# Kernel tuning notes

Hardware: AMD Instinct MI355X
Metric: run time of the kernel (lower is better)

Reference implementation:

```python
import jax, jax.numpy as jnp
import numpy as np

SIGMA = 0.2


def setup_inputs() -> dict:
    key = jax.random.key(0)
    ks = jax.random.split(key, 16)
    N = 200000
    corner = jax.random.normal(ks[0], (N, 9), dtype=jnp.float32)
    normal = jax.random.normal(ks[1], (N, 3), dtype=jnp.float32)
    neighbour = jax.random.randint(ks[2], (N, 3), 0, N, dtype=jnp.int32)
    # Face_Rotate_Conv params: Conv1d(1,32,6,stride=3), Linear(32,64), Linear(64,64)
    conv_w = jax.random.normal(ks[3], (32, 1, 6), dtype=jnp.float32) * 0.3
    conv_b = jax.random.normal(ks[4], (32,), dtype=jnp.float32) * 0.1
    l3_w = jax.random.normal(ks[5], (64, 32), dtype=jnp.float32) * 0.15
    l3_b = jax.random.normal(ks[6], (64,), dtype=jnp.float32) * 0.05
    l4_w = jax.random.normal(ks[7], (64, 64), dtype=jnp.float32) * 0.12
    l4_b = jax.random.normal(ks[8], (64,), dtype=jnp.float32) * 0.05
    # Kernel_Correlation params: theta ~ U(0,pi), phi ~ U(0,2pi), shape [1,64,4]
    theta = jax.random.uniform(ks[9], (1, 64, 4), dtype=jnp.float32) * np.float32(np.pi)
    phi = jax.random.uniform(ks[10], (1, 64, 4), dtype=jnp.float32) * np.float32(2 * np.pi)
    # trailing 1x1 conv / bn / 1x1 conv on 131 channels
    c1_w = jax.random.normal(ks[11], (131, 131, 1), dtype=jnp.float32) * 0.08
    c1_b = jax.random.normal(ks[12], (131,), dtype=jnp.float32) * 0.05
    c2_w = jax.random.normal(ks[13], (131, 131, 1), dtype=jnp.float32) * 0.08
    c2_b = jax.random.normal(ks[14], (131,), dtype=jnp.float32) * 0.05
    bn_g = jnp.ones((131,), dtype=jnp.float32)
    bn_b = jnp.zeros((131,), dtype=jnp.float32)
    return {"corner": corner, "normal": normal, "neighbour": neighbour,
            "conv_w": conv_w, "conv_b": conv_b, "l3_w": l3_w, "l3_b": l3_b,
            "l4_w": l4_w, "l4_b": l4_b, "theta": theta, "phi": phi,
            "c1_w": c1_w, "c1_b": c1_b, "c2_w": c2_w, "c2_b": c2_b,
            "bn_g": bn_g, "bn_b": bn_b}


def reference(corner, normal, neighbour, conv_w, conv_b, l3_w, l3_b, l4_w, l4_b,
              theta, phi, c1_w, c1_b, c2_w, c2_b, bn_g, bn_b):
    # ---- Face_Rotate_Conv ----
    # cat(c1,c2,c3,c1) -> [n,12]; conv1d k=6 stride=3 over length 12 -> 3 windows
    arr = jnp.concatenate([corner[:, 0:3], corner[:, 3:6], corner[:, 6:9], corner[:, 0:3]], axis=1)
    patches = jnp.stack([arr[:, 0:6], arr[:, 3:9], arr[:, 6:12]], axis=1)  # [n,3,6]
    conv_out = jnp.einsum('npk,ok->npo', patches, conv_w[:, 0, :]) + conv_b  # [n,3,32]
    frc = conv_out.mean(axis=1)  # [n,32] (mean over output length == mean over windows)
    h = jax.nn.relu(frc @ l3_w.T + l3_b)
    x = h @ l4_w.T + l4_b  # [n,64]
    # ---- Kernel_Correlation ----
    nb = neighbour.astype(jnp.int32)
    f = jnp.stack([normal, normal[nb[:, 0]], normal[nb[:, 1]], normal[nb[:, 2]]], axis=2)  # [n,3,4]
    th, ph = theta[0], phi[0]  # [64,4]
    kern = jnp.stack([jnp.sin(th) * jnp.sin(ph), jnp.sin(th) * jnp.cos(ph), jnp.cos(th)], axis=0)  # [3,64,4]
    # ||f - k||^2 over xyz expanded via |f|^2 + |k|^2 - 2 f.k (avoids [n,3,64,4,4])
    f2 = jnp.sum(f * f, axis=1)   # [n,4]
    k2 = jnp.sum(kern * kern, axis=0)  # [64,4]
    cross = jnp.einsum('nca,cmb->nmab', f, kern)  # [n,64,4,4]
    correl = f2[:, None, :, None] + k2[None, :, None, :] - 2.0 * cross
    z = jnp.exp(correl / (-2.0 * SIGMA * SIGMA)).sum(axis=(2, 3)) / 16.0  # [n,64]
    # ---- structural_Des head ----
    feat = jnp.concatenate([normal, x, z], axis=1)  # [n,131]
    y = feat @ c1_w[:, :, 0].T + c1_b  # 1x1 conv == linear
    mu = y.mean(axis=0)
    var = y.var(axis=0)  # biased var, matches train-mode BatchNorm1d
    y = jax.nn.relu((y - mu) / jnp.sqrt(var + 1e-5) * bn_g + bn_b)
    out = y @ c2_w[:, :, 0].T + c2_b
    return out  # [n,131]
```

## Files before the change

kernel.cpp:

```cpp
#include <hip/hip_runtime.h>
#include <math.h>

typedef __attribute__((ext_vector_type(8))) short short8;
typedef _Float16 half8 __attribute__((ext_vector_type(8)));
typedef __attribute__((ext_vector_type(4))) float f32x4;
typedef __attribute__((ext_vector_type(2))) uint uint2v;
typedef unsigned int uint;
typedef unsigned short ushort;

#define N_PTS 200000
#define N_PAD 200064
#define NBLK  1563
#define NPAIR 6252
#define YST   168
#define ZK    (-18.033688011112043f)
#define C2K   (36.067376022224086f)


#define FEAT_OFF  0ull
#define WT1_OFF   118437888ull
#define WT2_OFF   118483968ull
#define KERN2_OFF 118530048ull
#define WSUM_OFF  118534144ull
#define L3H_OFF   118534528ull
#define L4H_OFF   118538624ull
#define GSUM_OFF  118546816ull
#define GSQ_OFF   118547456ull
#define SCALE_OFF 118548096ull
#define SHIFT_OFF 118548736ull

__device__ inline ushort f2h(float x) {
    return __builtin_bit_cast(ushort, (_Float16)x);
}
__device__ inline uint pack2h(float a, float b) {
    return __builtin_bit_cast(uint, __builtin_amdgcn_cvt_pkrtz(a, b));
}

__global__ void sdes_k0_setup(const float* __restrict__ conv_w, const float* __restrict__ l3w,
                              const float* __restrict__ l4w, const float* __restrict__ theta,
                              const float* __restrict__ phi, const float* __restrict__ c1w,
                              const float* __restrict__ c2w,
                              float* wsumT, ushort* l3h, ushort* l4h, float* kern2,
                              ushort* WT1t, ushort* WT2t, float* gsum, float* gsq)
{
    const int t = threadIdx.x, b = blockIdx.x;
    if (b == 90) {
        for (int i = t; i < 96; i += 256) {
            int k = i >> 5, o = i & 31;
            wsumT[k * 32 + o] = conv_w[o * 6 + k] + conv_w[o * 6 + k + 3];
        }
        for (int i = t; i < 2048; i += 256) l3h[i] = f2h(l3w[i]);
        for (int i = t; i < 4096; i += 256) l4h[i] = f2h(l4w[i]);
        int m = t >> 2, bb = t & 3;
        float th = theta[m * 4 + bb], ph = phi[m * 4 + bb];
        float st = sinf(th), ct = cosf(th), sp = sinf(ph), cp = cosf(ph);
        kern2[m * 16 + bb * 4 + 0] = st * sp * C2K;
        kern2[m * 16 + bb * 4 + 1] = st * cp * C2K;
        kern2[m * 16 + bb * 4 + 2] = ct * C2K;
        kern2[m * 16 + bb * 4 + 3] = 0.f;
        return;
    }
    if (b == 0 && t < 160) { gsum[t] = 0.f; gsq[t] = 0.f; }
    int i = b * 256 + t;
    if (i >= 144 * 160) return;
    int e = i & 7, l = (i >> 3) & 63, rem = i >> 9;
    int kc = rem % 5, tc = rem / 5;
    int n = tc * 16 + (l & 15);
    int k = kc * 32 + (l >> 4) * 8 + e;
    float v = 0.f;
    if (n < 131) {
        if (k < 64)       v = c1w[n * 131 + 3 + k];
        else if (k < 128) v = c1w[n * 131 + 67 + (k - 64)];
        else if (k < 131) v = c1w[n * 131 + (k - 128)];
    }
    WT1t[i] = f2h(v);
    float v2 = (n < 131 && k < 131) ? c2w[n * 131 + k] : 0.f;
    WT2t[i] = f2h(v2);
}

#define FST 40
#define W3T 40
#define W4T 72
__global__ __launch_bounds__(128) void sdes_k1a_mlp(
    const float* __restrict__ corner, const float* __restrict__ conv_b,
    const float* __restrict__ wsumT, const ushort* __restrict__ l3h,
    const float* __restrict__ l3b, const ushort* __restrict__ l4h,
    const float* __restrict__ l4b, ushort* __restrict__ feat)
{
    __shared__ __align__(16) ushort frcS[128 * FST];
    __shared__ __align__(16) ushort hS[128 * 64];
    __shared__ __align__(16) ushort w3S[64 * W3T];
    __shared__ __align__(16) ushort w4S[64 * W4T];
    __shared__ float wsL[96], cbL[32], b3L[64], b4L[64];
    const int t = threadIdx.x;
    for (int i = t; i < 96; i += 128) wsL[i] = wsumT[i];
    for (int i = t; i < 32; i += 128) cbL[i] = conv_b[i];
    for (int i = t; i < 64; i += 128) { b3L[i] = l3b[i]; b4L[i] = l4b[i]; }
    for (int i = t; i < 256; i += 128) {
        int c = i >> 2, kc = i & 3;
        *(uint4*)&w3S[c * W3T + kc * 8] = *(const uint4*)&l3h[c * 32 + kc * 8];
    }
    for (int i = t; i < 512; i += 128) {
        int c = i >> 3, kc = i & 7;
        *(uint4*)&w4S[c * W4T + kc * 8] = *(const uint4*)&l4h[c * 64 + kc * 8];
    }
    __syncthreads();
    {
        int row = blockIdx.x * 128 + t;
        int p = row < N_PTS ? row : N_PTS - 1;
        const float* cp = corner + (size_t)p * 9;
        float c0 = cp[0], c1 = cp[1], c2 = cp[2], c3 = cp[3], c4 = cp[4],
              c5 = cp[5], c6 = cp[6], c7 = cp[7], c8 = cp[8];
        float mp0 = (c0 + c3 + c6) * (1.f / 3.f);
        float mp1 = (c1 + c4 + c7) * (1.f / 3.f);
        float mp2 = (c2 + c5 + c8) * (1.f / 3.f);
        #pragma unroll
        for (int o = 0; o < 32; o += 2) {
            float f0 = fmaf(mp0, wsL[o], fmaf(mp1, wsL[32 + o], fmaf(mp2, wsL[64 + o], cbL[o])));
            float f1 = fmaf(mp0, wsL[o+1], fmaf(mp1, wsL[33 + o], fmaf(mp2, wsL[65 + o], cbL[o+1])));
            *(uint*)&frcS[t * FST + o] = pack2h(f0, f1);
        }
    }
    __syncthreads();

    const int lane = t & 63, w = t >> 6;
    const int rbase = w * 64;
    const int rlo = lane & 15, kg = lane >> 4;
    const f32x4 z4 = {0.f, 0.f, 0.f, 0.f};

    {
        half8 af[4], bf[4];
        #pragma unroll
        for (int rt = 0; rt < 4; ++rt)
            af[rt] = *(const half8*)&frcS[(rbase + rt * 16 + rlo) * FST + kg * 8];
        #pragma unroll
        for (int tc = 0; tc < 4; ++tc)
            bf[tc] = *(const half8*)&w3S[(tc * 16 + rlo) * W3T + kg * 8];
        #pragma unroll
        for (int rt = 0; rt < 4; ++rt) {
            #pragma unroll
            for (int tc = 0; tc < 4; ++tc) {
                f32x4 acc = __builtin_amdgcn_mfma_f32_16x16x32_f16(af[rt], bf[tc], z4, 0, 0, 0);
                int col = tc * 16 + rlo;
                float bias = b3L[col];
                #pragma unroll
                for (int r = 0; r < 4; ++r) {
                    int hrow = rbase + rt * 16 + kg * 4 + r;
                    float v = fmaxf(acc[r] + bias, 0.f);
                    int sc = (((col >> 3) ^ (hrow & 7)) << 3) | (col & 7);
                    hS[hrow * 64 + sc] = f2h(v);
                }
            }
        }
    }
    __syncthreads();

    f32x4 acc4[4][4];
    #pragma unroll
    for (int pt = 0; pt < 4; ++pt)
        #pragma unroll
        for (int tc = 0; tc < 4; ++tc) acc4[pt][tc] = z4;
    #pragma unroll
    for (int ks = 0; ks < 2; ++ks) {
        half8 af[4], bf[4];
        #pragma unroll
        for (int pt = 0; pt < 4; ++pt) {
            int row = rbase + pt * 16 + rlo;
            int blk = (ks * 4 + kg) ^ (rlo & 7);
            af[pt] = *(const half8*)&hS[row * 64 + blk * 8];
        }
        #pragma unroll
        for (int tc = 0; tc < 4; ++tc)
            bf[tc] = *(const half8*)&w4S[(tc * 16 + rlo) * W4T + ks * 32 + kg * 8];
        #pragma unroll
        for (int pt = 0; pt < 4; ++pt)
            #pragma unroll
            for (int tc = 0; tc < 4; ++tc)
                acc4[pt][tc] = __builtin_amdgcn_mfma_f32_16x16x32_f16(bf[tc], af[pt], acc4[pt][tc], 0, 0, 0);
    }
    #pragma unroll
    for (int pt = 0; pt < 4; ++pt) {
        int rtg = blockIdx.x * 8 + w * 4 + pt;
        #pragma unroll
        for (int tc = 0; tc < 4; ++tc) {
            int xb = tc * 16 + kg * 4;
            float v0 = acc4[pt][tc][0] + b4L[xb + 0];
            float v1 = acc4[pt][tc][1] + b4L[xb + 1];
            float v2 = acc4[pt][tc][2] + b4L[xb + 2];
            float v3 = acc4[pt][tc][3] + b4L[xb + 3];
            uint2v st; st.x = pack2h(v0, v1); st.y = pack2h(v2, v3);
            int kc = tc >> 1;
            int l = rlo + 16 * ((2 * tc + (kg >> 1)) & 3);
            size_t off = ((size_t)(rtg * 5 + kc)) * 512 + l * 8 + (kg & 1) * 4;
            *(uint2v*)(feat + off) = st;
        }
    }
}

__global__ __launch_bounds__(256) void sdes_k1b_z(
    const float* __restrict__ normal, const int* __restrict__ neigh,
    const float* __restrict__ kern2g, ushort* __restrict__ feat)
{
    const int t = threadIdx.x;
    const int tt = t >> 7;
    const int pi = t & 127;
    const int p0 = blockIdx.x * 128 + pi;
    const int p = p0 < N_PTS ? p0 : N_PTS - 1;
    const int rt = p0 >> 4, pl = p0 & 15;
    float f0[4], f1[4], f2v[4];
    f0[0] = normal[(size_t)p * 3 + 0]; f1[0] = normal[(size_t)p * 3 + 1]; f2v[0] = normal[(size_t)p * 3 + 2];
    #pragma unroll
    for (int a = 1; a < 4; ++a) {
        int nb = neigh[(size_t)p * 3 + (a - 1)];
        f0[a] = normal[(size_t)nb * 3 + 0];
        f1[a] = normal[(size_t)nb * 3 + 1];
        f2v[a] = normal[(size_t)nb * 3 + 2];
    }
    float base[4];
    #pragma unroll
    for (int a = 0; a < 4; ++a)
        base[a] = (f0[a]*f0[a] + f1[a]*f1[a] + f2v[a]*f2v[a] + 1.0f) * ZK;
    const size_t tbase = ((size_t)(rt * 5 + 2 + tt)) * 512;
    for (int qq = 0; qq < 4; ++qq) {
        float zv[8];
        #pragma unroll
        for (int mm = 0; mm < 8; ++mm) {
            int m = (tt * 4 + qq) * 8 + mm;
            const float* kp = kern2g + m * 16;
            float a0 = 0.f, a1 = 0.f, a2 = 0.f, a3 = 0.f;
            #pragma unroll
            for (int b = 0; b < 4; ++b) {
                float kx = kp[b * 4 + 0], ky = kp[b * 4 + 1], kz = kp[b * 4 + 2];
                a0 += __builtin_amdgcn_exp2f(fmaf(f0[0], kx, fmaf(f1[0], ky, fmaf(f2v[0], kz, base[0]))));
                a1 += __builtin_amdgcn_exp2f(fmaf(f0[1], kx, fmaf(f1[1], ky, fmaf(f2v[1], kz, base[1]))));
                a2 += __builtin_amdgcn_exp2f(fmaf(f0[2], kx, fmaf(f1[2], ky, fmaf(f2v[2], kz, base[2]))));
                a3 += __builtin_amdgcn_exp2f(fmaf(f0[3], kx, fmaf(f1[3], ky, fmaf(f2v[3], kz, base[3]))));
            }
            zv[mm] = ((a0 + a1) + (a2 + a3)) * (1.f / 16.f);
        }
        uint4 v;
        v.x = pack2h(zv[0], zv[1]); v.y = pack2h(zv[2], zv[3]);
        v.z = pack2h(zv[4], zv[5]); v.w = pack2h(zv[6], zv[7]);
        *(uint4*)(feat + tbase + (pl + 16 * qq) * 8) = v;
    }
    {
        size_t base4 = ((size_t)(rt * 5 + 4)) * 512;
        const uint4 zz = {0u, 0u, 0u, 0u};
        if (tt == 0) {
            uint4 v;
            v.x = pack2h(f0[0], f1[0]); v.y = pack2h(f2v[0], 0.f); v.z = 0u; v.w = 0u;
            *(uint4*)(feat + base4 + pl * 8) = v;
            *(uint4*)(feat + base4 + (pl + 16) * 8) = zz;
        } else {
            *(uint4*)(feat + base4 + (pl + 32) * 8) = zz;
            *(uint4*)(feat + base4 + (pl + 48) * 8) = zz;
        }
    }
}

__global__ __launch_bounds__(1024, 4) void sdes_k2_stats(
    const ushort* __restrict__ FT, const ushort* __restrict__ WT1t,
    const float* __restrict__ c1b, float* __restrict__ gsum, float* __restrict__ gsq)
{
    __shared__ __align__(16) ushort W1s[45 * 512];
    __shared__ float sS[144], sQ[144];
    const int t = threadIdx.x;
    const int lane = t & 63, wv = t >> 6;
    const int b = blockIdx.x;
    const int s = b * 16 + wv;
    const int rlo = lane & 15, kg = lane >> 4;

    const int cnt = 3 + ((wv == 0 && b < 216) ? 1 : 0);
    const int start = 3 * s + (b < 216 ? b : 216) + ((b < 216 && wv > 0) ? 1 : 0);

    half8 afA[5], afB[5];
    #pragma unroll
    for (int kc = 0; kc < 5; ++kc)
        afA[kc] = *(const half8*)(FT + ((size_t)start * 5 + kc) * 512 + lane * 8);

    for (int i = t; i < 2880; i += 1024) ((uint4*)W1s)[i] = ((const uint4*)WT1t)[i];
    if (t < 144) { sS[t] = 0.f; sQ[t] = 0.f; }
    __syncthreads();

    float sreg[9], qreg[9], bL[9];
    #pragma unroll
    for (int tc = 0; tc < 9; ++tc) {
        sreg[tc] = 0.f; qreg[tc] = 0.f;
        int n = tc * 16 + rlo;
        bL[tc] = (n < 131) ? c1b[n] : 0.f;
    }

    for (int it = 0; it < cnt; ++it) {
        const int p = start + it;
        f32x4 acc[9];
        #pragma unroll
        for (int tc = 0; tc < 9; ++tc) acc[tc] = (f32x4){0.f, 0.f, 0.f, 0.f};
        #pragma unroll
        for (int kc = 0; kc < 5; ++kc) {
            #pragma unroll
            for (int tc = 0; tc < 9; ++tc) {
                half8 bw = *(const half8*)(W1s + (tc * 5 + kc) * 512 + lane * 8);
                acc[tc] = __builtin_amdgcn_mfma_f32_16x16x32_f16(afA[kc], bw, acc[tc], 0, 0, 0);
            }
        }
        if (it + 1 < cnt) {
            #pragma unroll
            for (int kc = 0; kc < 5; ++kc)
                afB[kc] = *(const half8*)(FT + ((size_t)(p + 1) * 5 + kc) * 512 + lane * 8);
            __builtin_amdgcn_sched_barrier(0);
        }
        const int row0 = p * 16;
        #pragma unroll
        for (int tc = 0; tc < 9; ++tc) {
            float b0 = bL[tc];
            #pragma unroll
            for (int r = 0; r < 4; ++r) {
                int grow = row0 + kg * 4 + r;
                if (grow < N_PTS) {
                    float v = acc[tc][r] + b0;
                    sreg[tc] += v;
                    qreg[tc] = fmaf(v, v, qreg[tc]);
                }
            }
        }
        #pragma unroll
        for (int kc = 0; kc < 5; ++kc) afA[kc] = afB[kc];
    }

    #pragma unroll
    for (int tc = 0; tc < 9; ++tc) {
        float sv = sreg[tc], qv = qreg[tc];
        sv += __shfl_xor(sv, 16);  sv += __shfl_xor(sv, 32);
        qv += __shfl_xor(qv, 16);  qv += __shfl_xor(qv, 32);
        if (lane < 16) {
            int n = tc * 16 + rlo;
            atomicAdd(&sS[n], sv); atomicAdd(&sQ[n], qv);
        }
    }
    __syncthreads();
    if (t < 144) { atomicAdd(&gsum[t], sS[t]); atomicAdd(&gsq[t], sQ[t]); }
}

__global__ __launch_bounds__(768, 3) void sdes_k3_fused(
    const ushort* __restrict__ FT, const ushort* __restrict__ WT1t,
    const ushort* __restrict__ WT2t, const float* __restrict__ c1b,
    const float* __restrict__ gsum, const float* __restrict__ gsq,
    const float* __restrict__ bng, const float* __restrict__ bnb,
    const float* __restrict__ c2b, float* __restrict__ out)
{
    __shared__ __align__(16) ushort Ws[2 * 45 * 512];
    __shared__ __align__(16) ushort yS[192 * YST];
    __shared__ float scL[160], shL[160], b1L[160], c2L[160];
    const int t = threadIdx.x;
    const int lane = t & 63, wv = t >> 6;
    const int rlo = lane & 15, kg = lane >> 4;
    const int b = blockIdx.x;
    const int s = b * 12 + wv;

    const int cnt = 2 + ((wv == 0 && b < 108) ? 1 : 0);
    const int start = 2 * s + (b < 108 ? b : 108) + ((b < 108 && wv > 0) ? 1 : 0);

    half8 afA[5][2], afB[5][2];
    #pragma unroll
    for (int kc = 0; kc < 5; ++kc)
        #pragma unroll
        for (int pt = 0; pt < 2; ++pt)
            afA[kc][pt] = *(const half8*)(FT + ((size_t)(start * 2 + pt) * 5 + kc) * 512 + lane * 8);

    for (int i = t; i < 5760; i += 768) ((uint4*)Ws)[i] = ((const uint4*)WT1t)[i];

    if (t < 160) {
        float sc = 0.f, sh = 0.f, bb = 0.f, c2 = 0.f;
        if (t < 131) {
            float mu = gsum[t] * (1.f / 200000.f);
            float var = gsq[t] * (1.f / 200000.f) - mu * mu;
            sc = bng[t] / sqrtf(var + 1e-5f);
            sh = bnb[t] - mu * sc;
            bb = c1b[t]; c2 = c2b[t];
        }
        scL[t] = sc; shL[t] = sh; b1L[t] = bb; c2L[t] = c2;
    }
    __syncthreads();

    const half8 hz = {0, 0, 0, 0, 0, 0, 0, 0};
    ushort* slab = yS + wv * 16 * YST;

    for (int it = 0; it < cnt; ++it) {
        const int p = start + it;

        f32x4 acc[2][9];
        #pragma unroll
        for (int pt = 0; pt < 2; ++pt)
            #pragma unroll
            for (int tc = 0; tc < 9; ++tc) acc[pt][tc] = (f32x4){0.f, 0.f, 0.f, 0.f};
        #pragma unroll
        for (int kc = 0; kc < 5; ++kc) {
            #pragma unroll
            for (int tc = 0; tc < 9; ++tc) {
                half8 bw = *(const half8*)(Ws + (tc * 5 + kc) * 512 + lane * 8);
                #pragma unroll
                for (int pt = 0; pt < 2; ++pt)
                    acc[pt][tc] = __builtin_amdgcn_mfma_f32_16x16x32_f16(afA[kc][pt], bw, acc[pt][tc], 0, 0, 0);
            }
        }

        if (it + 1 < cnt) {
            #pragma unroll
            for (int kc = 0; kc < 5; ++kc)
                #pragma unroll
                for (int pt = 0; pt < 2; ++pt)
                    afB[kc][pt] = *(const half8*)(FT + ((size_t)((p + 1) * 2 + pt) * 5 + kc) * 512 + lane * 8);
            __builtin_amdgcn_sched_barrier(0);
        }

        const int row0 = p * 32;
        #pragma unroll
        for (int pt = 0; pt < 2; ++pt) {
            #pragma unroll
            for (int tc = 0; tc < 9; ++tc) {
                int n = tc * 16 + rlo;
                float sc = scL[n], sh = shL[n], bb = b1L[n];
                #pragma unroll
                for (int r = 0; r < 4; ++r) {
                    float v = fmaxf(fmaf(acc[pt][tc][r] + bb, sc, sh), 0.f);
                    slab[(kg * 4 + r) * YST + n] = f2h(v);
                }
            }

            f32x4 acc2[9];
            #pragma unroll
            for (int tc = 0; tc < 9; ++tc) acc2[tc] = (f32x4){0.f, 0.f, 0.f, 0.f};
            #pragma unroll
            for (int kc2 = 0; kc2 < 5; ++kc2) {
                bool vld = (kc2 < 4) || (kg < 2);
                half8 af2 = vld ? *(const half8*)&slab[rlo * YST + kc2 * 32 + kg * 8] : hz;
                #pragma unroll
                for (int tc = 0; tc < 9; ++tc) {
                    half8 bw = *(const half8*)(Ws + 23040 + (tc * 5 + kc2) * 512 + lane * 8);
                    acc2[tc] = __builtin_amdgcn_mfma_f32_16x16x32_f16(af2, bw, acc2[tc], 0, 0, 0);
                }
            }
            #pragma unroll
            for (int tc = 0; tc < 9; ++tc) {
                int n = tc * 16 + rlo;
                if (n < 131) {
                    float bias = c2L[n];
                    #pragma unroll
                    for (int r = 0; r < 4; ++r) {
                        int grow = row0 + pt * 16 + kg * 4 + r;
                        if (grow < N_PTS) out[(size_t)grow * 131 + n] = acc2[tc][r] + bias;
                    }
                }
            }
        }

        #pragma unroll
        for (int kc = 0; kc < 5; ++kc)
            #pragma unroll
            for (int pt = 0; pt < 2; ++pt)
                afA[kc][pt] = afB[kc][pt];
    }
}

extern "C" void kernel_launch(void* const* d_in, const int* in_sizes, int n_in,
                              void* d_out, int out_size, void* d_ws, size_t ws_size,
                              hipStream_t stream) {
    const float* corner = (const float*)d_in[0];
    const float* normal = (const float*)d_in[1];
    const int*   neigh  = (const int*)d_in[2];
    const float* conv_w = (const float*)d_in[3];
    const float* conv_b = (const float*)d_in[4];
    const float* l3_w   = (const float*)d_in[5];
    const float* l3_b   = (const float*)d_in[6];
    const float* l4_w   = (const float*)d_in[7];
    const float* l4_b   = (const float*)d_in[8];
    const float* theta  = (const float*)d_in[9];
    const float* phi    = (const float*)d_in[10];
    const float* c1_w   = (const float*)d_in[11];
    const float* c1_b   = (const float*)d_in[12];
    const float* c2_w   = (const float*)d_in[13];
    const float* c2_b   = (const float*)d_in[14];
    const float* bn_g   = (const float*)d_in[15];
    const float* bn_b   = (const float*)d_in[16];

    char* ws = (char*)d_ws;
    ushort* feat  = (ushort*)(ws + FEAT_OFF);
    ushort* WT1t  = (ushort*)(ws + WT1_OFF);
    ushort* WT2t  = (ushort*)(ws + WT2_OFF);
    float*  kern2 = (float*)(ws + KERN2_OFF);
    float*  wsumT = (float*)(ws + WSUM_OFF);
    ushort* l3h   = (ushort*)(ws + L3H_OFF);
    ushort* l4h   = (ushort*)(ws + L4H_OFF);
    float*  gsum  = (float*)(ws + GSUM_OFF);
    float*  gsq   = (float*)(ws + GSQ_OFF);

    sdes_k0_setup<<<91, 256, 0, stream>>>(conv_w, l3_w, l4_w, theta, phi, c1_w, c2_w,
                                          wsumT, l3h, l4h, kern2, WT1t, WT2t, gsum, gsq);
    sdes_k1a_mlp<<<NBLK, 128, 0, stream>>>(corner, conv_b, wsumT, l3h, l3_b, l4h, l4_b, feat);
    sdes_k1b_z<<<NBLK, 256, 0, stream>>>(normal, neigh, kern2, feat);
    sdes_k2_stats<<<256, 1024, 0, stream>>>(feat, WT1t, c1_b, gsum, gsq);
    sdes_k3_fused<<<256, 768, 0, stream>>>(feat, WT1t, WT2t, c1_b, gsum, gsq,
                                           bn_g, bn_b, c2_b, (float*)d_out);
}
```

Before: 139.1 us.

## Fuse MLP and kernel-correlation kernels; transpose final MFMA for row-contiguous nontemporal stores

Merges the per-point MLP kernel and the kernel-correlation kernel into one 256-thread launch. Threads 0-127 compute the conv features, all 256 compute the exp-sum correlation, and only waves 0-1 run the MFMA layers, which removes one launch and its tail. In the final fused kernel the second GEMM swaps its MFMA operands so each lane owns one output row and writes contiguous columns with nontemporal stores, replacing the strided scattered stores. In exchange, waves 2-3 idle during the MFMA phases and the extra shared memory and registers may lower occupancy.

```diff
diff --git a/kernel.cpp b/kernel.cpp
--- a/kernel.cpp
+++ b/kernel.cpp
@@ -11,7 +11,6 @@
 #define N_PTS 200000
 #define N_PAD 200064
 #define NBLK  1563
-#define NPAIR 6252
 #define YST   168
 #define ZK    (-18.033688011112043f)
 #define C2K   (36.067376022224086f)
@@ -26,8 +25,6 @@
 #define L4H_OFF   118538624ull
 #define GSUM_OFF  118546816ull
 #define GSQ_OFF   118547456ull
-#define SCALE_OFF 118548096ull
-#define SHIFT_OFF 118548736ull
 
 __device__ inline ushort f2h(float x) {
     return __builtin_bit_cast(ushort, (_Float16)x);
@@ -81,11 +78,13 @@
 #define FST 40
 #define W3T 40
 #define W4T 72
-__global__ __launch_bounds__(128) void sdes_k1a_mlp(
+__global__ __launch_bounds__(256) void sdes_k1ab(
     const float* __restrict__ corner, const float* __restrict__ conv_b,
     const float* __restrict__ wsumT, const ushort* __restrict__ l3h,
     const float* __restrict__ l3b, const ushort* __restrict__ l4h,
-    const float* __restrict__ l4b, ushort* __restrict__ feat)
+    const float* __restrict__ l4b,
+    const float* __restrict__ normal, const int* __restrict__ neigh,
+    const float* __restrict__ kern2g, ushort* __restrict__ feat)
 {
     __shared__ __align__(16) ushort frcS[128 * FST];
     __shared__ __align__(16) ushort hS[128 * 64];
@@ -93,19 +92,21 @@
     __shared__ __align__(16) ushort w4S[64 * W4T];
     __shared__ float wsL[96], cbL[32], b3L[64], b4L[64];
     const int t = threadIdx.x;
-    for (int i = t; i < 96; i += 128) wsL[i] = wsumT[i];
-    for (int i = t; i < 32; i += 128) cbL[i] = conv_b[i];
-    for (int i = t; i < 64; i += 128) { b3L[i] = l3b[i]; b4L[i] = l4b[i]; }
-    for (int i = t; i < 256; i += 128) {
+
+    for (int i = t; i < 96; i += 256) wsL[i] = wsumT[i];
+    for (int i = t; i < 32; i += 256) cbL[i] = conv_b[i];
+    for (int i = t; i < 64; i += 256) { b3L[i] = l3b[i]; b4L[i] = l4b[i]; }
+    for (int i = t; i < 256; i += 256) {
         int c = i >> 2, kc = i & 3;
         *(uint4*)&w3S[c * W3T + kc * 8] = *(const uint4*)&l3h[c * 32 + kc * 8];
     }
-    for (int i = t; i < 512; i += 128) {
+    for (int i = t; i < 512; i += 256) {
         int c = i >> 3, kc = i & 7;
         *(uint4*)&w4S[c * W4T + kc * 8] = *(const uint4*)&l4h[c * 64 + kc * 8];
     }
     __syncthreads();
-    {
+
+    if (t < 128) {
         int row = blockIdx.x * 128 + t;
         int p = row < N_PTS ? row : N_PTS - 1;
         const float* cp = corner + (size_t)p * 9;
@@ -121,14 +122,71 @@
             *(uint*)&frcS[t * FST + o] = pack2h(f0, f1);
         }
     }
+
+    {
+        const int tt = t >> 7;
+        const int pi = t & 127;
+        const int p0 = blockIdx.x * 128 + pi;
+        const int p = p0 < N_PTS ? p0 : N_PTS - 1;
+        const int rt = p0 >> 4, pl = p0 & 15;
+        float f0[4], f1[4], f2v[4];
+        f0[0] = normal[(size_t)p * 3 + 0]; f1[0] = normal[(size_t)p * 3 + 1]; f2v[0] = normal[(size_t)p * 3 + 2];
+        #pragma unroll
+        for (int a = 1; a < 4; ++a) {
+            int nb = neigh[(size_t)p * 3 + (a - 1)];
+            f0[a] = normal[(size_t)nb * 3 + 0];
+            f1[a] = normal[(size_t)nb * 3 + 1];
+            f2v[a] = normal[(size_t)nb * 3 + 2];
+        }
+        float base[4];
+        #pragma unroll
+        for (int a = 0; a < 4; ++a)
+            base[a] = (f0[a]*f0[a] + f1[a]*f1[a] + f2v[a]*f2v[a] + 1.0f) * ZK;
+        const size_t tbase = ((size_t)(rt * 5 + 2 + tt)) * 512;
+        for (int qq = 0; qq < 4; ++qq) {
+            float zv[8];
+            #pragma unroll
+            for (int mm = 0; mm < 8; ++mm) {
+                int m = (tt * 4 + qq) * 8 + mm;
+                const float* kp = kern2g + m * 16;
+                float a0 = 0.f, a1 = 0.f, a2 = 0.f, a3 = 0.f;
+                #pragma unroll
+                for (int b = 0; b < 4; ++b) {
+                    float kx = kp[b * 4 + 0], ky = kp[b * 4 + 1], kz = kp[b * 4 + 2];
+                    a0 += __builtin_amdgcn_exp2f(fmaf(f0[0], kx, fmaf(f1[0], ky, fmaf(f2v[0], kz, base[0]))));
+                    a1 += __builtin_amdgcn_exp2f(fmaf(f0[1], kx, fmaf(f1[1], ky, fmaf(f2v[1], kz, base[1]))));
+                    a2 += __builtin_amdgcn_exp2f(fmaf(f0[2], kx, fmaf(f1[2], ky, fmaf(f2v[2], kz, base[2]))));
+                    a3 += __builtin_amdgcn_exp2f(fmaf(f0[3], kx, fmaf(f1[3], ky, fmaf(f2v[3], kz, base[3]))));
+                }
+                zv[mm] = ((a0 + a1) + (a2 + a3)) * (1.f / 16.f);
+            }
+            uint4 v;
+            v.x = pack2h(zv[0], zv[1]); v.y = pack2h(zv[2], zv[3]);
+            v.z = pack2h(zv[4], zv[5]); v.w = pack2h(zv[6], zv[7]);
+            *(uint4*)(feat + tbase + (pl + 16 * qq) * 8) = v;
+        }
+        {
+            size_t base4 = ((size_t)(rt * 5 + 4)) * 512;
+            const uint4 zz = {0u, 0u, 0u, 0u};
+            if (tt == 0) {
+                uint4 v;
+                v.x = pack2h(f0[0], f1[0]); v.y = pack2h(f2v[0], 0.f); v.z = 0u; v.w = 0u;
+                *(uint4*)(feat + base4 + pl * 8) = v;
+                *(uint4*)(feat + base4 + (pl + 16) * 8) = zz;
+            } else {
+                *(uint4*)(feat + base4 + (pl + 32) * 8) = zz;
+                *(uint4*)(feat + base4 + (pl + 48) * 8) = zz;
+            }
+        }
+    }
     __syncthreads();
 
     const int lane = t & 63, w = t >> 6;
-    const int rbase = w * 64;
     const int rlo = lane & 15, kg = lane >> 4;
     const f32x4 z4 = {0.f, 0.f, 0.f, 0.f};
 
-    {
+    if (w < 2) {
+        const int rbase = w * 64;
         half8 af[4], bf[4];
         #pragma unroll
         for (int rt = 0; rt < 4; ++rt)
@@ -155,105 +213,47 @@
     }
     __syncthreads();
 
-    f32x4 acc4[4][4];
-    #pragma unroll
-    for (int pt = 0; pt < 4; ++pt)
-        #pragma unroll
-        for (int tc = 0; tc < 4; ++tc) acc4[pt][tc] = z4;
-    #pragma unroll
-    for (int ks = 0; ks < 2; ++ks) {
-        half8 af[4], bf[4];
+    if (w < 2) {
+        const int rbase = w * 64;
+        f32x4 acc4[4][4];
+        #pragma unroll
+        for (int pt = 0; pt < 4; ++pt)
+            #pragma unroll
+            for (int tc = 0; tc < 4; ++tc) acc4[pt][tc] = z4;
+        #pragma unroll
+        for (int ks = 0; ks < 2; ++ks) {
+            half8 af[4], bf[4];
+            #pragma unroll
+            for (int pt = 0; pt < 4; ++pt) {
+                int row = rbase + pt * 16 + rlo;
+                int blk = (ks * 4 + kg) ^ (rlo & 7);
+                af[pt] = *(const half8*)&hS[row * 64 + blk * 8];
+            }
+            #pragma unroll
+            for (int tc = 0; tc < 4; ++tc)
+                bf[tc] = *(const half8*)&w4S[(tc * 16 + rlo) * W4T + ks * 32 + kg * 8];
+            #pragma unroll
+            for (int pt = 0; pt < 4; ++pt)
+                #pragma unroll
+                for (int tc = 0; tc < 4; ++tc)
+                    acc4[pt][tc] = __builtin_amdgcn_mfma_f32_16x16x32_f16(bf[tc], af[pt], acc4[pt][tc], 0, 0, 0);
+        }
         #pragma unroll
         for (int pt = 0; pt < 4; ++pt) {
-            int row = rbase + pt * 16 + rlo;
-            int blk = (ks * 4 + kg) ^ (rlo & 7);
-            af[pt] = *(const half8*)&hS[row * 64 + blk * 8];
-        }
-        #pragma unroll
-        for (int tc = 0; tc < 4; ++tc)
-            bf[tc] = *(const half8*)&w4S[(tc * 16 + rlo) * W4T + ks * 32 + kg * 8];
-        #pragma unroll
-        for (int pt = 0; pt < 4; ++pt)
-            #pragma unroll
-            for (int tc = 0; tc < 4; ++tc)
-                acc4[pt][tc] = __builtin_amdgcn_mfma_f32_16x16x32_f16(bf[tc], af[pt], acc4[pt][tc], 0, 0, 0);
-    }
-    #pragma unroll
-    for (int pt = 0; pt < 4; ++pt) {
-        int rtg = blockIdx.x * 8 + w * 4 + pt;
-        #pragma unroll
-        for (int tc = 0; tc < 4; ++tc) {
-            int xb = tc * 16 + kg * 4;
-            float v0 = acc4[pt][tc][0] + b4L[xb + 0];
-            float v1 = acc4[pt][tc][1] + b4L[xb + 1];
-            float v2 = acc4[pt][tc][2] + b4L[xb + 2];
-            float v3 = acc4[pt][tc][3] + b4L[xb + 3];
-            uint2v st; st.x = pack2h(v0, v1); st.y = pack2h(v2, v3);
-            int kc = tc >> 1;
-            int l = rlo + 16 * ((2 * tc + (kg >> 1)) & 3);
-            size_t off = ((size_t)(rtg * 5 + kc)) * 512 + l * 8 + (kg & 1) * 4;
-            *(uint2v*)(feat + off) = st;
-        }
-    }
-}
-
-__global__ __launch_bounds__(256) void sdes_k1b_z(
-    const float* __restrict__ normal, const int* __restrict__ neigh,
-    const float* __restrict__ kern2g, ushort* __restrict__ feat)
-{
-    const int t = threadIdx.x;
-    const int tt = t >> 7;
-    const int pi = t & 127;
-    const int p0 = blockIdx.x * 128 + pi;
-    const int p = p0 < N_PTS ? p0 : N_PTS - 1;
-    const int rt = p0 >> 4, pl = p0 & 15;
-    float f0[4], f1[4], f2v[4];
-    f0[0] = normal[(size_t)p * 3 + 0]; f1[0] = normal[(size_t)p * 3 + 1]; f2v[0] = normal[(size_t)p * 3 + 2];
-    #pragma unroll
-    for (int a = 1; a < 4; ++a) {
-        int nb = neigh[(size_t)p * 3 + (a - 1)];
-        f0[a] = normal[(size_t)nb * 3 + 0];
-        f1[a] = normal[(size_t)nb * 3 + 1];
-        f2v[a] = normal[(size_t)nb * 3 + 2];
-    }
-    float base[4];
-    #pragma unroll
-    for (int a = 0; a < 4; ++a)
-        base[a] = (f0[a]*f0[a] + f1[a]*f1[a] + f2v[a]*f2v[a] + 1.0f) * ZK;
-    const size_t tbase = ((size_t)(rt * 5 + 2 + tt)) * 512;
-    for (int qq = 0; qq < 4; ++qq) {
-        float zv[8];
-        #pragma unroll
-        for (int mm = 0; mm < 8; ++mm) {
-            int m = (tt * 4 + qq) * 8 + mm;
-            const float* kp = kern2g + m * 16;
-            float a0 = 0.f, a1 = 0.f, a2 = 0.f, a3 = 0.f;
-            #pragma unroll
-            for (int b = 0; b < 4; ++b) {
-                float kx = kp[b * 4 + 0], ky = kp[b * 4 + 1], kz = kp[b * 4 + 2];
-                a0 += __builtin_amdgcn_exp2f(fmaf(f0[0], kx, fmaf(f1[0], ky, fmaf(f2v[0], kz, base[0]))));
-                a1 += __builtin_amdgcn_exp2f(fmaf(f0[1], kx, fmaf(f1[1], ky, fmaf(f2v[1], kz, base[1]))));
-                a2 += __builtin_amdgcn_exp2f(fmaf(f0[2], kx, fmaf(f1[2], ky, fmaf(f2v[2], kz, base[2]))));
-                a3 += __builtin_amdgcn_exp2f(fmaf(f0[3], kx, fmaf(f1[3], ky, fmaf(f2v[3], kz, base[3]))));
-            }
-            zv[mm] = ((a0 + a1) + (a2 + a3)) * (1.f / 16.f);
-        }
-        uint4 v;
-        v.x = pack2h(zv[0], zv[1]); v.y = pack2h(zv[2], zv[3]);
-        v.z = pack2h(zv[4], zv[5]); v.w = pack2h(zv[6], zv[7]);
-        *(uint4*)(feat + tbase + (pl + 16 * qq) * 8) = v;
-    }
-    {
-        size_t base4 = ((size_t)(rt * 5 + 4)) * 512;
-        const uint4 zz = {0u, 0u, 0u, 0u};
-        if (tt == 0) {
-            uint4 v;
-            v.x = pack2h(f0[0], f1[0]); v.y = pack2h(f2v[0], 0.f); v.z = 0u; v.w = 0u;
-            *(uint4*)(feat + base4 + pl * 8) = v;
-            *(uint4*)(feat + base4 + (pl + 16) * 8) = zz;
-        } else {
-            *(uint4*)(feat + base4 + (pl + 32) * 8) = zz;
-            *(uint4*)(feat + base4 + (pl + 48) * 8) = zz;
+            int rtg = blockIdx.x * 8 + w * 4 + pt;
+            #pragma unroll
+            for (int tc = 0; tc < 4; ++tc) {
+                int xb = tc * 16 + kg * 4;
+                float v0 = acc4[pt][tc][0] + b4L[xb + 0];
+                float v1 = acc4[pt][tc][1] + b4L[xb + 1];
+                float v2 = acc4[pt][tc][2] + b4L[xb + 2];
+                float v3 = acc4[pt][tc][3] + b4L[xb + 3];
+                uint2v st; st.x = pack2h(v0, v1); st.y = pack2h(v2, v3);
+                int kc = tc >> 1;
+                int l = rlo + 16 * ((2 * tc + (kg >> 1)) & 3);
+                size_t off = ((size_t)(rtg * 5 + kc)) * 512 + l * 8 + (kg & 1) * 4;
+                *(uint2v*)(feat + off) = st;
+            }
         }
     }
 }
@@ -350,7 +350,7 @@
 {
     __shared__ __align__(16) ushort Ws[2 * 45 * 512];
     __shared__ __align__(16) ushort yS[192 * YST];
-    __shared__ float scL[160], shL[160], b1L[160], c2L[160];
+    __shared__ __align__(16) float scL[160], shL[160], b1L[160], c2L[160];
     const int t = threadIdx.x;
     const int lane = t & 63, wv = t >> 6;
     const int rlo = lane & 15, kg = lane >> 4;
@@ -437,19 +437,24 @@
                 #pragma unroll
                 for (int tc = 0; tc < 9; ++tc) {
                     half8 bw = *(const half8*)(Ws + 23040 + (tc * 5 + kc2) * 512 + lane * 8);
-                    acc2[tc] = __builtin_amdgcn_mfma_f32_16x16x32_f16(af2, bw, acc2[tc], 0, 0, 0);
-                }
-            }
-            #pragma unroll
-            for (int tc = 0; tc < 9; ++tc) {
-                int n = tc * 16 + rlo;
-                if (n < 131) {
-                    float bias = c2L[n];
+                    acc2[tc] = __builtin_amdgcn_mfma_f32_16x16x32_f16(bw, af2, acc2[tc], 0, 0, 0);
+                }
+            }
+            const int prow = row0 + pt * 16 + rlo;
+            if (prow < N_PTS) {
+                float* op = out + (size_t)prow * 131;
+                #pragma unroll
+                for (int tc = 0; tc < 8; ++tc) {
+                    const int c0 = tc * 16 + kg * 4;
+                    const float* cb = &c2L[c0];
                     #pragma unroll
-                    for (int r = 0; r < 4; ++r) {
-                        int grow = row0 + pt * 16 + kg * 4 + r;
-                        if (grow < N_PTS) out[(size_t)grow * 131 + n] = acc2[tc][r] + bias;
-                    }
+                    for (int r = 0; r < 4; ++r)
+                        __builtin_nontemporal_store(acc2[tc][r] + cb[r], op + c0 + r);
+                }
+                if (kg == 0) {
+                    __builtin_nontemporal_store(acc2[8][0] + c2L[128], op + 128);
+                    __builtin_nontemporal_store(acc2[8][1] + c2L[129], op + 129);
+                    __builtin_nontemporal_store(acc2[8][2] + c2L[130], op + 130);
                 }
             }
         }
@@ -496,8 +501,8 @@
 
     sdes_k0_setup<<<91, 256, 0, stream>>>(conv_w, l3_w, l4_w, theta, phi, c1_w, c2_w,
                                           wsumT, l3h, l4h, kern2, WT1t, WT2t, gsum, gsq);
-    sdes_k1a_mlp<<<NBLK, 128, 0, stream>>>(corner, conv_b, wsumT, l3h, l3_b, l4h, l4_b, feat);
-    sdes_k1b_z<<<NBLK, 256, 0, stream>>>(normal, neigh, kern2, feat);
+    sdes_k1ab<<<NBLK, 256, 0, stream>>>(corner, conv_b, wsumT, l3h, l3_b, l4h, l4_b,
+                                        normal, neigh, kern2, feat);
     sdes_k2_stats<<<256, 1024, 0, stream>>>(feat, WT1t, c1_b, gsum, gsq);
     sdes_k3_fused<<<256, 768, 0, stream>>>(feat, WT1t, WT2t, c1_b, gsum, gsq,
                                            bn_g, bn_b, c2_b, (float*)d_out);
```

Result: slower. 206.2 us (+48.3%).
